# Optimization experiments

Measured on AMD Instinct MI355X. Metric: run time of the kernel, lower is better.

## Reference

```python
import jax, jax.numpy as jnp
import numpy as np

B, T, C, K, D, N, ITERS = 16384, 8, 16, 4, 16, 16, 3


def setup_inputs() -> dict:
    key = jax.random.key(0)
    ks = jax.random.split(key, 12)
    rn = lambda k, s, sc=0.1: jax.random.normal(k, s, jnp.float32) * sc
    return {
        'frames': jax.random.uniform(ks[0], (B, T, 1, 16, 16), jnp.float32),
        'enc_w': rn(ks[1], (C, 1, 4, 4)), 'enc_b': jnp.zeros((C,), jnp.float32),
        'ln_w': jnp.ones((C,), jnp.float32), 'ln_b': jnp.zeros((C,), jnp.float32),
        'slot_mu': rn(ks[2], (1, K, D)),
        'wq': rn(ks[3], (D, D)), 'wk': rn(ks[4], (D, C)), 'wv': rn(ks[5], (D, C)),
        'gru_wih': rn(ks[6], (3 * D, D)), 'gru_whh': rn(ks[7], (3 * D, D)),
        'gru_bih': jnp.zeros((3 * D,), jnp.float32), 'gru_bhh': jnp.zeros((3 * D,), jnp.float32),
        's2s_w': rn(ks[8], (C * 16, D)), 's2s_b': jnp.zeros((C * 16,), jnp.float32),
        'mix_w': rn(ks[9], (C, K * C)), 'mix_b': jnp.zeros((C,), jnp.float32),
        'dec_w': rn(ks[10], (C, 1, 4, 4)), 'dec_b': jnp.zeros((1,), jnp.float32),
    }


def reference(frames, enc_w, enc_b, ln_w, ln_b, slot_mu, wq, wk, wv,
              gru_wih, gru_whh, gru_bih, gru_bhh, s2s_w, s2s_b,
              mix_w, mix_b, dec_w, dec_b):
    Bv, Tv = frames.shape[0], frames.shape[1]
    scale = D ** (-0.5)

    def layernorm(x):
        mu = jnp.mean(x, -1, keepdims=True)
        var = jnp.mean(jnp.square(x - mu), -1, keepdims=True)
        return (x - mu) * jax.lax.rsqrt(var + 1e-5) * ln_w + ln_b

    def gru_cell(x, h):  # torch GRUCell semantics, x,h: [M, D]
        gi = x @ gru_wih.T + gru_bih
        gh = h @ gru_whh.T + gru_bhh
        ir, iz, inn = jnp.split(gi, 3, axis=-1)
        hr, hz, hn = jnp.split(gh, 3, axis=-1)
        r = jax.nn.sigmoid(ir + hr)
        z = jax.nn.sigmoid(iz + hz)
        n = jnp.tanh(inn + r * hn)
        return (1.0 - z) * n + z * h

    def step(slots, frame):  # frame: [B,1,16,16]
        # encoder: conv k4 s4 -> [B,C,4,4], exact (erf) GELU as in torch default
        f = jax.lax.conv_general_dilated(frame, enc_w, (4, 4), 'VALID')
        f = jax.nn.gelu(f + enc_b[None, :, None, None], approximate=False)
        feat = f.reshape(Bv, C, N).transpose(0, 2, 1)  # [B,N,C]
        x = layernorm(feat)
        kk = x @ wk.T  # [B,N,D]
        vv = x @ wv.T
        s = slots
        for _ in range(ITERS):
            q = s @ wq.T                                  # [B,K,D]
            attn = jnp.einsum('bkd,bnd->bkn', q, kk) * scale
            attn = jax.nn.softmax(attn, axis=1)           # softmax over slots
            upd = jnp.einsum('bkn,bnd->bkd', attn, vv)
            s = gru_cell(upd.reshape(-1, D), s.reshape(-1, D)).reshape(Bv, K, D)
        spat = s @ s2s_w.T + s2s_b                        # [B,K,C*16]
        mixed = spat.reshape(Bv, K * C, 4, 4)
        mixed = jnp.einsum('oc,bchw->bohw', mix_w, mixed) + mix_b[None, :, None, None]
        # transposed conv k4 s4 (non-overlapping): each input pixel -> 4x4 block
        pred = jnp.einsum('bcij,code->boidje', mixed, dec_w).reshape(Bv, 1, 16, 16)
        pred = jax.nn.sigmoid(pred + dec_b[None, :, None, None])
        return s, pred

    slots0 = jnp.broadcast_to(slot_mu, (Bv, K, D))
    xs = jnp.swapaxes(frames[:, 1:Tv - 1], 0, 1)  # [T-2, B, 1, 16, 16]
    _, preds = jax.lax.scan(step, slots0, xs)
    return jnp.swapaxes(preds, 0, 1)  # [B, T-2, 1, 16, 16]
```

## Files before the change

kernel.cpp:

```cpp
#include <hip/hip_runtime.h>

#define TH 256
#define BATCHES_PB 8

typedef float f32x2 __attribute__((ext_vector_type(2)));

__device__ __forceinline__ f32x2 mk2(float a, float b) { f32x2 r; r.x = a; r.y = b; return r; }
__device__ __forceinline__ f32x2 pkfma(f32x2 a, f32x2 b, f32x2 c) {
  asm("v_pk_fma_f32 %0, %1, %2, %3" : "=v"(c) : "v"(a), "v"(b), "0"(c));
  return c;
}
__device__ __forceinline__ f32x2 pkfma_blo(f32x2 a, f32x2 b, f32x2 c) {
  asm("v_pk_fma_f32 %0, %1, %2, %3 op_sel_hi:[1,0,1]" : "=v"(c) : "v"(a), "v"(b), "0"(c));
  return c;
}
__device__ __forceinline__ f32x2 pkfma_bhi(f32x2 a, f32x2 b, f32x2 c) {
  asm("v_pk_fma_f32 %0, %1, %2, %3 op_sel:[0,1,0] op_sel_hi:[1,1,1]" : "=v"(c) : "v"(a), "v"(b), "0"(c));
  return c;
}

__device__ __forceinline__ float sigm(float x) {
  return __fdividef(1.0f, 1.0f + __expf(-x));
}
__device__ __forceinline__ float fast_tanh(float x) {
  float ex = __expf(2.0f * x);
  return 1.0f - __fdividef(2.0f, ex + 1.0f);
}
__device__ __forceinline__ float gelu_erf(float a) {
  float z = fabsf(a) * 0.70710678118654752440f;
  float t = __fdividef(1.0f, __builtin_fmaf(0.3275911f, z, 1.0f));
  float p = __builtin_fmaf(1.061405429f, t, -1.453152027f);
  p = __builtin_fmaf(p, t, 1.421413741f);
  p = __builtin_fmaf(p, t, -0.284496736f);
  p = __builtin_fmaf(p, t, 0.254829592f);
  p = p * t;
  float e = __expf(-z * z);
  float y = __builtin_fmaf(-p, e, 1.0f);
  return 0.5f * a * (1.0f + copysignf(y, a));
}

#define WAVE_SYNC() asm volatile("s_waitcnt lgkmcnt(0)" ::: "memory")

__device__ __forceinline__ void ldrow(const float* __restrict__ p, f32x2* w) {
  float4 a = *(const float4*)(p);
  float4 b = *(const float4*)(p + 4);
  float4 c = *(const float4*)(p + 8);
  float4 d = *(const float4*)(p + 12);
  w[0]=mk2(a.x,a.y); w[1]=mk2(a.z,a.w); w[2]=mk2(b.x,b.y); w[3]=mk2(b.z,b.w);
  w[4]=mk2(c.x,c.y); w[5]=mk2(c.z,c.w); w[6]=mk2(d.x,d.y); w[7]=mk2(d.z,d.w);
}
__device__ __forceinline__ float dotr(const f32x2* w, const f32x2* x, float bias) {
  f32x2 a = mk2(bias, 0.f), b = mk2(0.f, 0.f);
  a = pkfma(w[0], x[0], a); b = pkfma(w[1], x[1], b);
  a = pkfma(w[2], x[2], a); b = pkfma(w[3], x[3], b);
  a = pkfma(w[4], x[4], a); b = pkfma(w[5], x[5], b);
  a = pkfma(w[6], x[6], a); b = pkfma(w[7], x[7], b);
  f32x2 s = a + b;
  return s.x + s.y;
}

__global__ void prep_kernel(const float* __restrict__ s2s_w, const float* __restrict__ s2s_b,
                            const float* __restrict__ mix_w, const float* __restrict__ mix_b,
                            const float* __restrict__ dec_w, const float* __restrict__ dec_b,
                            float* __restrict__ M2T, float* __restrict__ C0) {
  const int pix = threadIdx.x;
  const int I = pix >> 4, J = pix & 15;
  const int i = I >> 2, dd = I & 3, j = J >> 2, ee = J & 3;
  const int p = i*4 + j, q = dd*4 + ee;
  float DWrow[64];
  for (int kc = 0; kc < 64; ++kc) {
    float a = 0.f;
    for (int o = 0; o < 16; ++o) a += dec_w[o*16 + q] * mix_w[o*64 + kc];
    DWrow[kc] = a;
  }
  float c0 = dec_b[0];
  for (int o = 0; o < 16; ++o) c0 += dec_w[o*16 + q] * mix_b[o];
  for (int k = 0; k < 4; ++k)
    for (int c = 0; c < 16; ++c) c0 += DWrow[k*16 + c] * s2s_b[c*16 + p];
  C0[pix] = c0;
  for (int k = 0; k < 4; ++k)
    for (int d = 0; d < 16; ++d) {
      float a = 0.f;
      for (int c = 0; c < 16; ++c) a += DWrow[k*16 + c] * s2s_w[(c*16 + p)*16 + d];
      M2T[(k*16 + d)*256 + pix] = a;
    }
}

__launch_bounds__(TH, 3)
__global__ void microslot_kernel(
    const float* __restrict__ frames,
    const float* __restrict__ enc_w, const float* __restrict__ enc_b,
    const float* __restrict__ ln_w,  const float* __restrict__ ln_b,
    const float* __restrict__ slot_mu,
    const float* __restrict__ wq, const float* __restrict__ wk, const float* __restrict__ wv,
    const float* __restrict__ wih, const float* __restrict__ whh,
    const float* __restrict__ bih, const float* __restrict__ bhh,
    const float* __restrict__ g_M2T, const float* __restrict__ g_C0,
    float* __restrict__ out)
{
  __shared__ __align__(16) float W_enc[16*20];
  __shared__ __align__(16) float W_qT[16*20];
  __shared__ __align__(16) float W_k[16*20];
  __shared__ __align__(16) float W_v[16*20];
  __shared__ __align__(16) float W_ih[48*20];
  __shared__ __align__(16) float W_hh[48*20];
  __shared__ float B_enc[16], LNW[16], LNB[16];
  __shared__ __align__(16) float svb[BATCHES_PB*68];
  __shared__ __align__(16) float SCR[4][2176];

  const int tid = threadIdx.x;

  { int idx = tid; if (idx < 256) W_enc[(idx>>4)*20 + (idx&15)] = enc_w[idx]; }
  { int idx = tid; if (idx < 256) W_qT[(idx&15)*20 + (idx>>4)] = wq[idx]; }
  { int idx = tid; if (idx < 256) W_k [(idx>>4)*20 + (idx&15)] = wk[idx]; }
  { int idx = tid; if (idx < 256) W_v [(idx>>4)*20 + (idx&15)] = wv[idx]; }
  for (int idx = tid; idx < 768; idx += TH) W_ih[(idx>>4)*20 + (idx&15)] = wih[idx];
  for (int idx = tid; idx < 768; idx += TH) W_hh[(idx>>4)*20 + (idx&15)] = whh[idx];
  if (tid < 16) { B_enc[tid] = enc_b[tid]; LNW[tid] = ln_w[tid]; LNB[tid] = ln_b[tid]; }
  __syncthreads();

  const int wid = tid >> 6, lane = tid & 63;
  const int ln = lane & 15, lg = lane >> 4;
  float* S = SCR[wid];
  constexpr int o_sbA = 0,    o_sbB = 64,  o_tmpA = 128, o_tmpB = 192;
  constexpr int o_xqA = 256,  o_xqB = 576, o_kkA = 896,  o_kkB = 1216;
  constexpr int o_vvA = 1536, o_vvB = 1856;

  float s_regA = slot_mu[lane];
  float s_regB = s_regA;
  const float bi_r = bih[ln], bi_z = bih[16+ln], bi_n = bih[32+ln];
  const float bh_r = bhh[ln], bh_z = bhh[16+ln], bh_n = bhh[32+ln];

  const int i0 = ln >> 2, j0 = ln & 3;
  const size_t bA = (size_t)(blockIdx.x * BATCHES_PB + wid*2);
  const float* fpA = frames + bA * 2048;
  const float* fpB = fpA + 2048;

  for (int st = 0; st < 6; ++st) {
    const int t = st + 1;
    f32x2 pA[8], pB[8];
    #pragma unroll
    for (int a = 0; a < 4; ++a) {
      float4 v = *(const float4*)(fpA + (size_t)t*256 + (4*i0 + a)*16 + 4*j0);
      pA[2*a] = mk2(v.x, v.y); pA[2*a+1] = mk2(v.z, v.w);
      float4 w = *(const float4*)(fpB + (size_t)t*256 + (4*i0 + a)*16 + 4*j0);
      pB[2*a] = mk2(w.x, w.y); pB[2*a+1] = mk2(w.z, w.w);
    }
    float xA[4], xB[4];
    #pragma unroll
    for (int cc = 0; cc < 4; ++cc) {
      int c = 4*lg + cc;
      f32x2 w[8]; ldrow(&W_enc[c*20], w);
      float be = B_enc[c];
      xA[cc] = gelu_erf(dotr(w, pA, be));
      xB[cc] = gelu_erf(dotr(w, pB, be));
    }
    float s1A = xA[0]+xA[1]+xA[2]+xA[3], s2A = xA[0]*xA[0]+xA[1]*xA[1]+xA[2]*xA[2]+xA[3]*xA[3];
    float s1B = xB[0]+xB[1]+xB[2]+xB[3], s2B = xB[0]*xB[0]+xB[1]*xB[1]+xB[2]*xB[2]+xB[3]*xB[3];
    s1A += __shfl_xor(s1A, 16); s1A += __shfl_xor(s1A, 32);
    s2A += __shfl_xor(s2A, 16); s2A += __shfl_xor(s2A, 32);
    s1B += __shfl_xor(s1B, 16); s1B += __shfl_xor(s1B, 32);
    s2B += __shfl_xor(s2B, 16); s2B += __shfl_xor(s2B, 32);
    float muA = s1A * 0.0625f, varA = s2A * 0.0625f - muA*muA, rsA = rsqrtf(varA + 1e-5f);
    float muB = s1B * 0.0625f, varB = s2B * 0.0625f - muB*muB, rsB = rsqrtf(varB + 1e-5f);
    #pragma unroll
    for (int cc = 0; cc < 4; ++cc) {
      int c = 4*lg + cc;
      xA[cc] = (xA[cc]-muA)*rsA*LNW[c] + LNB[c];
      xB[cc] = (xB[cc]-muB)*rsB*LNW[c] + LNB[c];
    }
    *(float4*)&S[o_xqA + ln*20 + 4*lg] = make_float4(xA[0],xA[1],xA[2],xA[3]);
    *(float4*)&S[o_xqB + ln*20 + 4*lg] = make_float4(xB[0],xB[1],xB[2],xB[3]);
    WAVE_SYNC();

    {
      f32x2 xrA[8], xrB[8];
      ldrow(&S[o_xqA + ln*20], xrA);
      ldrow(&S[o_xqB + ln*20], xrB);
      float kkA4[4], kkB4[4];
      #pragma unroll
      for (int cc = 0; cc < 4; ++cc) {
        int dd = 4*lg + cc;
        f32x2 w[8];
        ldrow(&W_k[dd*20], w);
        kkA4[cc] = dotr(w, xrA, 0.f);
        kkB4[cc] = dotr(w, xrB, 0.f);
        ldrow(&W_v[dd*20], w);
        S[o_vvA + dd*20 + ln] = dotr(w, xrA, 0.f);
        S[o_vvB + dd*20 + ln] = dotr(w, xrB, 0.f);
      }
      *(float4*)&S[o_kkA + ln*20 + 4*lg] = make_float4(kkA4[0],kkA4[1],kkA4[2],kkA4[3]);
      *(float4*)&S[o_kkB + ln*20 + 4*lg] = make_float4(kkB4[0],kkB4[1],kkB4[2],kkB4[3]);
    }
    WAVE_SYNC();

    f32x2 vvrA[8], vvrB[8];
    {
      f32x2 kA[8], kB[8];
      ldrow(&S[o_kkA + ln*20], kA);
      ldrow(&S[o_kkB + ln*20], kB);
      ldrow(&S[o_vvA + ln*20], vvrA);
      ldrow(&S[o_vvB + ln*20], vvrB);
      float kqA4[4], kqB4[4];
      #pragma unroll
      for (int cc = 0; cc < 4; ++cc) {
        f32x2 w[8]; ldrow(&W_qT[(4*lg+cc)*20], w);
        kqA4[cc] = dotr(w, kA, 0.f);
        kqB4[cc] = dotr(w, kB, 0.f);
      }
      *(float4*)&S[o_xqA + ln*20 + 4*lg] = make_float4(kqA4[0],kqA4[1],kqA4[2],kqA4[3]);
      *(float4*)&S[o_xqB + ln*20 + 4*lg] = make_float4(kqB4[0],kqB4[1],kqB4[2],kqB4[3]);
    }

    #pragma unroll 1
    for (int it = 0; it < 3; ++it) {
      S[o_sbA + lane] = s_regA;
      S[o_sbB + lane] = s_regB;
      WAVE_SYNC();
      f32x2 hrA[8], hrB[8];
      ldrow(&S[o_sbA + lg*16], hrA);
      ldrow(&S[o_sbB + lg*16], hrB);
      f32x2 kw[8];
      ldrow(&S[o_xqA + ln*20], kw);
      float lA = 0.25f * dotr(kw, hrA, 0.f);
      ldrow(&S[o_xqB + ln*20], kw);
      float lB = 0.25f * dotr(kw, hrB, 0.f);
      float eA = __expf(lA), eB = __expf(lB);
      float seA = eA + __shfl_xor(eA, 16); seA += __shfl_xor(seA, 32);
      float seB = eB + __shfl_xor(eB, 16); seB += __shfl_xor(seB, 32);
      S[o_tmpA + lane] = __fdividef(eA, seA);
      S[o_tmpB + lane] = __fdividef(eB, seB);
      WAVE_SYNC();
      f32x2 aA[8], aB[8];
      ldrow(&S[o_tmpA + lg*16], aA);
      ldrow(&S[o_tmpB + lg*16], aB);
      float uA = dotr(aA, vvrA, 0.f);
      float uB = dotr(aB, vvrB, 0.f);
      S[o_tmpA + lane] = uA;
      S[o_tmpB + lane] = uB;
      WAVE_SYNC();
      f32x2 urA[8], urB[8];
      ldrow(&S[o_tmpA + lg*16], urA);
      ldrow(&S[o_tmpB + lg*16], urB);
      f32x2 girA = mk2(bi_r,0.f), gizA = mk2(bi_z,0.f), ginA = mk2(bi_n,0.f);
      f32x2 ghrA = mk2(bh_r,0.f), ghzA = mk2(bh_z,0.f), ghnA = mk2(bh_n,0.f);
      f32x2 girB = mk2(bi_r,0.f), gizB = mk2(bi_z,0.f), ginB = mk2(bi_n,0.f);
      f32x2 ghrB = mk2(bh_r,0.f), ghzB = mk2(bh_z,0.f), ghnB = mk2(bh_n,0.f);
      #pragma unroll
      for (int qd = 0; qd < 4; ++qd) {
        float4 wr = *(const float4*)&W_ih[(   ln)*20 + 4*qd];
        float4 wz = *(const float4*)&W_ih[(16+ln)*20 + 4*qd];
        float4 wn = *(const float4*)&W_ih[(32+ln)*20 + 4*qd];
        float4 vr = *(const float4*)&W_hh[(   ln)*20 + 4*qd];
        float4 vz = *(const float4*)&W_hh[(16+ln)*20 + 4*qd];
        float4 vn = *(const float4*)&W_hh[(32+ln)*20 + 4*qd];
        f32x2 wrl = mk2(wr.x,wr.y), wrh = mk2(wr.z,wr.w);
        f32x2 wzl = mk2(wz.x,wz.y), wzh = mk2(wz.z,wz.w);
        f32x2 wnl = mk2(wn.x,wn.y), wnh = mk2(wn.z,wn.w);
        f32x2 vrl = mk2(vr.x,vr.y), vrh = mk2(vr.z,vr.w);
        f32x2 vzl = mk2(vz.x,vz.y), vzh = mk2(vz.z,vz.w);
        f32x2 vnl = mk2(vn.x,vn.y), vnh = mk2(vn.z,vn.w);
        girA = pkfma(wrl, urA[2*qd], girA); girA = pkfma(wrh, urA[2*qd+1], girA);
        girB = pkfma(wrl, urB[2*qd], girB); girB = pkfma(wrh, urB[2*qd+1], girB);
        gizA = pkfma(wzl, urA[2*qd], gizA); gizA = pkfma(wzh, urA[2*qd+1], gizA);
        gizB = pkfma(wzl, urB[2*qd], gizB); gizB = pkfma(wzh, urB[2*qd+1], gizB);
        ginA = pkfma(wnl, urA[2*qd], ginA); ginA = pkfma(wnh, urA[2*qd+1], ginA);
        ginB = pkfma(wnl, urB[2*qd], ginB); ginB = pkfma(wnh, urB[2*qd+1], ginB);
        ghrA = pkfma(vrl, hrA[2*qd], ghrA); ghrA = pkfma(vrh, hrA[2*qd+1], ghrA);
        ghrB = pkfma(vrl, hrB[2*qd], ghrB); ghrB = pkfma(vrh, hrB[2*qd+1], ghrB);
        ghzA = pkfma(vzl, hrA[2*qd], ghzA); ghzA = pkfma(vzh, hrA[2*qd+1], ghzA);
        ghzB = pkfma(vzl, hrB[2*qd], ghzB); ghzB = pkfma(vzh, hrB[2*qd+1], ghzB);
        ghnA = pkfma(vnl, hrA[2*qd], ghnA); ghnA = pkfma(vnh, hrA[2*qd+1], ghnA);
        ghnB = pkfma(vnl, hrB[2*qd], ghnB); ghnB = pkfma(vnh, hrB[2*qd+1], ghnB);
      }
      {
        float rg = sigm((girA.x+girA.y) + (ghrA.x+ghrA.y));
        float zg = sigm((gizA.x+gizA.y) + (ghzA.x+ghzA.y));
        float nh = fast_tanh((ginA.x+ginA.y) + rg*(ghnA.x+ghnA.y));
        s_regA = (1.f - zg)*nh + zg*s_regA;
      }
      {
        float rg = sigm((girB.x+girB.y) + (ghrB.x+ghrB.y));
        float zg = sigm((gizB.x+gizB.y) + (ghzB.x+ghzB.y));
        float nh = fast_tanh((ginB.x+ginB.y) + rg*(ghnB.x+ghnB.y));
        s_regB = (1.f - zg)*nh + zg*s_regB;
      }
    }

    svb[(wid*2+0)*68 + lane] = s_regA;
    svb[(wid*2+1)*68 + lane] = s_regB;
    __syncthreads();
    {
      const int rb = tid >> 5, c32 = tid & 31;
      const float* svp = &svb[rb*68];
      const int pix1 = 4*c32, pix2 = pix1 + 128;
      const float* m1p = g_M2T + pix1;
      const float* m2p = g_M2T + pix2;
      float4 c01 = *(const float4*)(g_C0 + pix1);
      float4 c02 = *(const float4*)(g_C0 + pix2);
      f32x2 a01 = mk2(c01.x, c01.y), a23 = mk2(c01.z, c01.w);
      f32x2 b01 = mk2(c02.x, c02.y), b23 = mk2(c02.z, c02.w);
      #pragma unroll 4
      for (int q4 = 0; q4 < 16; ++q4) {
        float4 sv = *(const float4*)(svp + 4*q4);
        f32x2 svA = mk2(sv.x, sv.y), svB = mk2(sv.z, sv.w);
        float4 m0 = *(const float4*)(m1p + (4*q4+0)*256);
        float4 m1 = *(const float4*)(m1p + (4*q4+1)*256);
        float4 m2 = *(const float4*)(m1p + (4*q4+2)*256);
        float4 m3 = *(const float4*)(m1p + (4*q4+3)*256);
        a01 = pkfma_blo(mk2(m0.x,m0.y), svA, a01); a23 = pkfma_blo(mk2(m0.z,m0.w), svA, a23);
        a01 = pkfma_bhi(mk2(m1.x,m1.y), svA, a01); a23 = pkfma_bhi(mk2(m1.z,m1.w), svA, a23);
        a01 = pkfma_blo(mk2(m2.x,m2.y), svB, a01); a23 = pkfma_blo(mk2(m2.z,m2.w), svB, a23);
        a01 = pkfma_bhi(mk2(m3.x,m3.y), svB, a01); a23 = pkfma_bhi(mk2(m3.z,m3.w), svB, a23);
        float4 n0 = *(const float4*)(m2p + (4*q4+0)*256);
        float4 n1 = *(const float4*)(m2p + (4*q4+1)*256);
        float4 n2 = *(const float4*)(m2p + (4*q4+2)*256);
        float4 n3 = *(const float4*)(m2p + (4*q4+3)*256);
        b01 = pkfma_blo(mk2(n0.x,n0.y), svA, b01); b23 = pkfma_blo(mk2(n0.z,n0.w), svA, b23);
        b01 = pkfma_bhi(mk2(n1.x,n1.y), svA, b01); b23 = pkfma_bhi(mk2(n1.z,n1.w), svA, b23);
        b01 = pkfma_blo(mk2(n2.x,n2.y), svB, b01); b23 = pkfma_blo(mk2(n2.z,n2.w), svB, b23);
        b01 = pkfma_bhi(mk2(n3.x,n3.y), svB, b01); b23 = pkfma_bhi(mk2(n3.z,n3.w), svB, b23);
      }
      const size_t ob = (size_t)(blockIdx.x*BATCHES_PB + rb)*(6*256) + (size_t)st*256;
      *(float4*)(out + ob + pix1) = make_float4(sigm(a01.x), sigm(a01.y), sigm(a23.x), sigm(a23.y));
      *(float4*)(out + ob + pix2) = make_float4(sigm(b01.x), sigm(b01.y), sigm(b23.x), sigm(b23.y));
    }
    __syncthreads();
  }
}

extern "C" void kernel_launch(void* const* d_in, const int* in_sizes, int n_in,
                              void* d_out, int out_size, void* d_ws, size_t ws_size,
                              hipStream_t stream) {
  const float* frames  = (const float*)d_in[0];
  const float* enc_w   = (const float*)d_in[1];
  const float* enc_b   = (const float*)d_in[2];
  const float* ln_w    = (const float*)d_in[3];
  const float* ln_b    = (const float*)d_in[4];
  const float* slot_mu = (const float*)d_in[5];
  const float* wq      = (const float*)d_in[6];
  const float* wk      = (const float*)d_in[7];
  const float* wv      = (const float*)d_in[8];
  const float* wih     = (const float*)d_in[9];
  const float* whh     = (const float*)d_in[10];
  const float* bih     = (const float*)d_in[11];
  const float* bhh     = (const float*)d_in[12];
  const float* s2s_w   = (const float*)d_in[13];
  const float* s2s_b   = (const float*)d_in[14];
  const float* mix_w   = (const float*)d_in[15];
  const float* mix_b   = (const float*)d_in[16];
  const float* dec_w   = (const float*)d_in[17];
  const float* dec_b   = (const float*)d_in[18];
  float* out = (float*)d_out;

  float* g_M2T = (float*)d_ws;
  float* g_C0  = g_M2T + 64*256;

  hipLaunchKernelGGL(prep_kernel, dim3(1), dim3(256), 0, stream,
                     s2s_w, s2s_b, mix_w, mix_b, dec_w, dec_b, g_M2T, g_C0);

  const int B = 16384;
  hipLaunchKernelGGL(microslot_kernel, dim3(B / BATCHES_PB), dim3(TH), 0, stream,
                     frames, enc_w, enc_b, ln_w, ln_b, slot_mu, wq, wk, wv,
                     wih, whh, bih, bhh, g_M2T, g_C0, out);
}
```

Measured before the change: 347.8 us.

## Fold Wq and Wk into a single precomputed matrix and shrink scratch for occupancy

A fused Wq^T·Wk matrix is precomputed in the prep kernel, so each frame needs one 16x16 projection to obtain keys already multiplied by the query weights instead of two chained projections. The projected keys stay in registers across the attention iterations rather than being reloaded from LDS. Per-wave scratch is compacted and launch bounds are raised from 3 to 4 blocks per SM to allow higher occupancy, with more register pressure as the cost. The decoder stage's thread-to-pixel mapping is also reorganised so that each wave covers a contiguous pixel range.

New measurement: 481.9 us. 38.5% more time.

```diff
diff --git a/kernel.cpp b/kernel.cpp
--- a/kernel.cpp
+++ b/kernel.cpp
@@ -62,8 +62,16 @@
 __global__ void prep_kernel(const float* __restrict__ s2s_w, const float* __restrict__ s2s_b,
                             const float* __restrict__ mix_w, const float* __restrict__ mix_b,
                             const float* __restrict__ dec_w, const float* __restrict__ dec_b,
-                            float* __restrict__ M2T, float* __restrict__ C0) {
+                            const float* __restrict__ wq,    const float* __restrict__ wk,
+                            float* __restrict__ M2T, float* __restrict__ C0,
+                            float* __restrict__ WKQ) {
   const int pix = threadIdx.x;
+  {
+    const int j = pix >> 4, c = pix & 15;
+    float a = 0.f;
+    for (int d = 0; d < 16; ++d) a += wq[d*16 + j] * wk[d*16 + c];
+    WKQ[pix] = a;
+  }
   const int I = pix >> 4, J = pix & 15;
   const int i = I >> 2, dd = I & 3, j = J >> 2, ee = J & 3;
   const int p = i*4 + j, q = dd*4 + ee;
@@ -86,34 +94,33 @@
     }
 }
 
-__launch_bounds__(TH, 3)
+__launch_bounds__(TH, 4)
 __global__ void microslot_kernel(
     const float* __restrict__ frames,
     const float* __restrict__ enc_w, const float* __restrict__ enc_b,
     const float* __restrict__ ln_w,  const float* __restrict__ ln_b,
     const float* __restrict__ slot_mu,
-    const float* __restrict__ wq, const float* __restrict__ wk, const float* __restrict__ wv,
+    const float* __restrict__ wv,
     const float* __restrict__ wih, const float* __restrict__ whh,
     const float* __restrict__ bih, const float* __restrict__ bhh,
     const float* __restrict__ g_M2T, const float* __restrict__ g_C0,
+    const float* __restrict__ g_WKQ,
     float* __restrict__ out)
 {
   __shared__ __align__(16) float W_enc[16*20];
-  __shared__ __align__(16) float W_qT[16*20];
-  __shared__ __align__(16) float W_k[16*20];
+  __shared__ __align__(16) float W_kq[16*20];
   __shared__ __align__(16) float W_v[16*20];
   __shared__ __align__(16) float W_ih[48*20];
   __shared__ __align__(16) float W_hh[48*20];
   __shared__ float B_enc[16], LNW[16], LNB[16];
   __shared__ __align__(16) float svb[BATCHES_PB*68];
-  __shared__ __align__(16) float SCR[4][2176];
+  __shared__ __align__(16) float SCR[4][1536];
 
   const int tid = threadIdx.x;
 
   { int idx = tid; if (idx < 256) W_enc[(idx>>4)*20 + (idx&15)] = enc_w[idx]; }
-  { int idx = tid; if (idx < 256) W_qT[(idx&15)*20 + (idx>>4)] = wq[idx]; }
-  { int idx = tid; if (idx < 256) W_k [(idx>>4)*20 + (idx&15)] = wk[idx]; }
-  { int idx = tid; if (idx < 256) W_v [(idx>>4)*20 + (idx&15)] = wv[idx]; }
+  { int idx = tid; if (idx < 256) W_kq [(idx>>4)*20 + (idx&15)] = g_WKQ[idx]; }
+  { int idx = tid; if (idx < 256) W_v  [(idx>>4)*20 + (idx&15)] = wv[idx]; }
   for (int idx = tid; idx < 768; idx += TH) W_ih[(idx>>4)*20 + (idx&15)] = wih[idx];
   for (int idx = tid; idx < 768; idx += TH) W_hh[(idx>>4)*20 + (idx&15)] = whh[idx];
   if (tid < 16) { B_enc[tid] = enc_b[tid]; LNW[tid] = ln_w[tid]; LNB[tid] = ln_b[tid]; }
@@ -122,9 +129,8 @@
   const int wid = tid >> 6, lane = tid & 63;
   const int ln = lane & 15, lg = lane >> 4;
   float* S = SCR[wid];
-  constexpr int o_sbA = 0,    o_sbB = 64,  o_tmpA = 128, o_tmpB = 192;
-  constexpr int o_xqA = 256,  o_xqB = 576, o_kkA = 896,  o_kkB = 1216;
-  constexpr int o_vvA = 1536, o_vvB = 1856;
+  constexpr int o_xqA = 0,    o_vvA = 320,  o_sbA = 640,  o_tmpA = 704;
+  constexpr int o_xqB = 768,  o_vvB = 1088, o_sbB = 1408, o_tmpB = 1472;
 
   float s_regA = slot_mu[lane];
   float s_regB = s_regA;
@@ -173,43 +179,31 @@
     *(float4*)&S[o_xqB + ln*20 + 4*lg] = make_float4(xB[0],xB[1],xB[2],xB[3]);
     WAVE_SYNC();
 
+    f32x2 vvrA[8], vvrB[8], kqrA[8], kqrB[8];
     {
       f32x2 xrA[8], xrB[8];
       ldrow(&S[o_xqA + ln*20], xrA);
       ldrow(&S[o_xqB + ln*20], xrB);
-      float kkA4[4], kkB4[4];
+      WAVE_SYNC();
+      float kqA4[4], kqB4[4];
       #pragma unroll
       for (int cc = 0; cc < 4; ++cc) {
         int dd = 4*lg + cc;
         f32x2 w[8];
-        ldrow(&W_k[dd*20], w);
-        kkA4[cc] = dotr(w, xrA, 0.f);
-        kkB4[cc] = dotr(w, xrB, 0.f);
+        ldrow(&W_kq[dd*20], w);
+        kqA4[cc] = dotr(w, xrA, 0.f);
+        kqB4[cc] = dotr(w, xrB, 0.f);
         ldrow(&W_v[dd*20], w);
         S[o_vvA + dd*20 + ln] = dotr(w, xrA, 0.f);
         S[o_vvB + dd*20 + ln] = dotr(w, xrB, 0.f);
       }
-      *(float4*)&S[o_kkA + ln*20 + 4*lg] = make_float4(kkA4[0],kkA4[1],kkA4[2],kkA4[3]);
-      *(float4*)&S[o_kkB + ln*20 + 4*lg] = make_float4(kkB4[0],kkB4[1],kkB4[2],kkB4[3]);
-    }
-    WAVE_SYNC();
-
-    f32x2 vvrA[8], vvrB[8];
-    {
-      f32x2 kA[8], kB[8];
-      ldrow(&S[o_kkA + ln*20], kA);
-      ldrow(&S[o_kkB + ln*20], kB);
+      *(float4*)&S[o_xqA + ln*20 + 4*lg] = make_float4(kqA4[0],kqA4[1],kqA4[2],kqA4[3]);
+      *(float4*)&S[o_xqB + ln*20 + 4*lg] = make_float4(kqB4[0],kqB4[1],kqB4[2],kqB4[3]);
+      WAVE_SYNC();
       ldrow(&S[o_vvA + ln*20], vvrA);
       ldrow(&S[o_vvB + ln*20], vvrB);
-      float kqA4[4], kqB4[4];
-      #pragma unroll
-      for (int cc = 0; cc < 4; ++cc) {
-        f32x2 w[8]; ldrow(&W_qT[(4*lg+cc)*20], w);
-        kqA4[cc] = dotr(w, kA, 0.f);
-        kqB4[cc] = dotr(w, kB, 0.f);
-      }
-      *(float4*)&S[o_xqA + ln*20 + 4*lg] = make_float4(kqA4[0],kqA4[1],kqA4[2],kqA4[3]);
-      *(float4*)&S[o_xqB + ln*20 + 4*lg] = make_float4(kqB4[0],kqB4[1],kqB4[2],kqB4[3]);
+      ldrow(&S[o_xqA + ln*20], kqrA);
+      ldrow(&S[o_xqB + ln*20], kqrB);
     }
 
     #pragma unroll 1
@@ -220,11 +214,8 @@
       f32x2 hrA[8], hrB[8];
       ldrow(&S[o_sbA + lg*16], hrA);
       ldrow(&S[o_sbB + lg*16], hrB);
-      f32x2 kw[8];
-      ldrow(&S[o_xqA + ln*20], kw);
-      float lA = 0.25f * dotr(kw, hrA, 0.f);
-      ldrow(&S[o_xqB + ln*20], kw);
-      float lB = 0.25f * dotr(kw, hrB, 0.f);
+      float lA = 0.25f * dotr(kqrA, hrA, 0.f);
+      float lB = 0.25f * dotr(kqrB, hrB, 0.f);
       float eA = __expf(lA), eB = __expf(lB);
       float seA = eA + __shfl_xor(eA, 16); seA += __shfl_xor(seA, 32);
       float seB = eB + __shfl_xor(eB, 16); seB += __shfl_xor(seB, 32);
@@ -291,39 +282,40 @@
     svb[(wid*2+1)*68 + lane] = s_regB;
     __syncthreads();
     {
-      const int rb = tid >> 5, c32 = tid & 31;
-      const float* svp = &svb[rb*68];
-      const int pix1 = 4*c32, pix2 = pix1 + 128;
+      const int u = lane & 7, r = lane >> 3;
+      const int pix0 = (wid << 6) + 4*u;
+      const int pix1 = pix0 + 32;
+      const float* svp = &svb[r*68];
+      const float* m0p = g_M2T + pix0;
       const float* m1p = g_M2T + pix1;
-      const float* m2p = g_M2T + pix2;
+      float4 c00 = *(const float4*)(g_C0 + pix0);
       float4 c01 = *(const float4*)(g_C0 + pix1);
-      float4 c02 = *(const float4*)(g_C0 + pix2);
-      f32x2 a01 = mk2(c01.x, c01.y), a23 = mk2(c01.z, c01.w);
-      f32x2 b01 = mk2(c02.x, c02.y), b23 = mk2(c02.z, c02.w);
+      f32x2 a01 = mk2(c00.x, c00.y), a23 = mk2(c00.z, c00.w);
+      f32x2 b01 = mk2(c01.x, c01.y), b23 = mk2(c01.z, c01.w);
       #pragma unroll 4
       for (int q4 = 0; q4 < 16; ++q4) {
         float4 sv = *(const float4*)(svp + 4*q4);
         f32x2 svA = mk2(sv.x, sv.y), svB = mk2(sv.z, sv.w);
-        float4 m0 = *(const float4*)(m1p + (4*q4+0)*256);
-        float4 m1 = *(const float4*)(m1p + (4*q4+1)*256);
-        float4 m2 = *(const float4*)(m1p + (4*q4+2)*256);
-        float4 m3 = *(const float4*)(m1p + (4*q4+3)*256);
+        float4 m0 = *(const float4*)(m0p + (4*q4+0)*256);
+        float4 m1 = *(const float4*)(m0p + (4*q4+1)*256);
+        float4 m2 = *(const float4*)(m0p + (4*q4+2)*256);
+        float4 m3 = *(const float4*)(m0p + (4*q4+3)*256);
         a01 = pkfma_blo(mk2(m0.x,m0.y), svA, a01); a23 = pkfma_blo(mk2(m0.z,m0.w), svA, a23);
         a01 = pkfma_bhi(mk2(m1.x,m1.y), svA, a01); a23 = pkfma_bhi(mk2(m1.z,m1.w), svA, a23);
         a01 = pkfma_blo(mk2(m2.x,m2.y), svB, a01); a23 = pkfma_blo(mk2(m2.z,m2.w), svB, a23);
         a01 = pkfma_bhi(mk2(m3.x,m3.y), svB, a01); a23 = pkfma_bhi(mk2(m3.z,m3.w), svB, a23);
-        float4 n0 = *(const float4*)(m2p + (4*q4+0)*256);
-        float4 n1 = *(const float4*)(m2p + (4*q4+1)*256);
-        float4 n2 = *(const float4*)(m2p + (4*q4+2)*256);
-        float4 n3 = *(const float4*)(m2p + (4*q4+3)*256);
+        float4 n0 = *(const float4*)(m1p + (4*q4+0)*256);
+        float4 n1 = *(const float4*)(m1p + (4*q4+1)*256);
+        float4 n2 = *(const float4*)(m1p + (4*q4+2)*256);
+        float4 n3 = *(const float4*)(m1p + (4*q4+3)*256);
         b01 = pkfma_blo(mk2(n0.x,n0.y), svA, b01); b23 = pkfma_blo(mk2(n0.z,n0.w), svA, b23);
         b01 = pkfma_bhi(mk2(n1.x,n1.y), svA, b01); b23 = pkfma_bhi(mk2(n1.z,n1.w), svA, b23);
         b01 = pkfma_blo(mk2(n2.x,n2.y), svB, b01); b23 = pkfma_blo(mk2(n2.z,n2.w), svB, b23);
         b01 = pkfma_bhi(mk2(n3.x,n3.y), svB, b01); b23 = pkfma_bhi(mk2(n3.z,n3.w), svB, b23);
       }
-      const size_t ob = (size_t)(blockIdx.x*BATCHES_PB + rb)*(6*256) + (size_t)st*256;
-      *(float4*)(out + ob + pix1) = make_float4(sigm(a01.x), sigm(a01.y), sigm(a23.x), sigm(a23.y));
-      *(float4*)(out + ob + pix2) = make_float4(sigm(b01.x), sigm(b01.y), sigm(b23.x), sigm(b23.y));
+      const size_t ob = (size_t)(blockIdx.x*BATCHES_PB + r)*(6*256) + (size_t)st*256;
+      *(float4*)(out + ob + pix0) = make_float4(sigm(a01.x), sigm(a01.y), sigm(a23.x), sigm(a23.y));
+      *(float4*)(out + ob + pix1) = make_float4(sigm(b01.x), sigm(b01.y), sigm(b23.x), sigm(b23.y));
     }
     __syncthreads();
   }
@@ -355,12 +347,14 @@
 
   float* g_M2T = (float*)d_ws;
   float* g_C0  = g_M2T + 64*256;
+  float* g_WKQ = g_C0 + 256;
 
   hipLaunchKernelGGL(prep_kernel, dim3(1), dim3(256), 0, stream,
-                     s2s_w, s2s_b, mix_w, mix_b, dec_w, dec_b, g_M2T, g_C0);
+                     s2s_w, s2s_b, mix_w, mix_b, dec_w, dec_b, wq, wk,
+                     g_M2T, g_C0, g_WKQ);
 
   const int B = 16384;
   hipLaunchKernelGGL(microslot_kernel, dim3(B / BATCHES_PB), dim3(TH), 0, stream,
-                     frames, enc_w, enc_b, ln_w, ln_b, slot_mu, wq, wk, wv,
-                     wih, whh, bih, bhh, g_M2T, g_C0, out);
-}
+                     frames, enc_w, enc_b, ln_w, ln_b, slot_mu, wv,
+                     wih, whh, bih, bhh, g_M2T, g_C0, g_WKQ, out);
+}
```
